# Optimization experiments

Measured on AMD Instinct MI355X. Metric: run time of the kernel, lower is better.

The kernel has to match this reference:

```python
import jax, jax.numpy as jnp
import numpy as np

S = 512          # number of scenes (sequences)
P = 128          # pedestrians per scene
G = 16           # groups per scene (labels 1..G, each of size P//G)
D_IN, D_HID, D_OUT, D_FINAL = 256, 512, 16, 64


def setup_inputs() -> dict:
    key = jax.random.key(0)
    ks = jax.random.split(key, 10)
    B = S * P
    h_states = jax.random.normal(ks[0], (B, D_IN), dtype=jnp.float32)
    end_pos = jax.random.normal(ks[1], (B, 2), dtype=jnp.float32)
    starts = jnp.arange(S, dtype=jnp.int64) * P
    seq_start_end = jnp.stack([starts, starts + P], axis=1)
    # labels 1..G within each scene; every group present -> n_group = G (static)
    end_group = ((jnp.arange(B, dtype=jnp.int64) % G) + 1).reshape(B, 1)
    s = 0.05  # scale randn params to keep activations tame
    W_intra_0 = s * jax.random.normal(ks[2], (D_IN, D_HID), dtype=jnp.float32)
    W_intra_1 = s * jax.random.normal(ks[3], (D_HID, D_OUT), dtype=jnp.float32)
    W_inter_0 = s * jax.random.normal(ks[4], (D_OUT, D_HID), dtype=jnp.float32)
    W_inter_1 = s * jax.random.normal(ks[5], (D_HID, D_OUT), dtype=jnp.float32)
    out_W = s * jax.random.normal(ks[6], (2 * D_OUT, D_FINAL), dtype=jnp.float32)
    out_b = jnp.zeros((D_FINAL,), dtype=jnp.float32)
    return {"h_states": h_states, "end_pos": end_pos,
            "seq_start_end": seq_start_end, "end_group": end_group,
            "W_intra_0": W_intra_0, "W_intra_1": W_intra_1,
            "W_inter_0": W_inter_0, "W_inter_1": W_inter_1,
            "out_W": out_W, "out_b": out_b}


def reference(h_states, end_pos, seq_start_end, end_group,
              W_intra_0, W_intra_1, W_inter_0, W_inter_1, out_W, out_b):
    B = h_states.shape[0]
    num_seq = seq_start_end.shape[0]
    P_ = B // num_seq
    labels = end_group.reshape(num_seq, P_)
    h_seq = h_states.reshape(num_seq, P_, -1)
    eye = jnp.eye(P_, dtype=bool)
    grp_ids = jnp.arange(1, G + 1)

    def per_scene(h, lab):
        # intra-group adjacency: same nonzero group, plus self loops
        M = ((lab[:, None] == lab[None, :]) & (lab[:, None] != 0)) | eye
        Mf = M.astype(h.dtype)
        A = Mf / jnp.sum(Mf, axis=1, keepdims=True)          # row-normalize
        H = jax.nn.relu((A @ h) @ W_intra_0)
        H_intra = jax.nn.relu((A @ H) @ W_intra_1)           # (P, D_OUT)
        # GPool: unique rows of M == one-hot group membership (all labels nonzero)
        onehot = (lab[None, :] == grp_ids[:, None]).astype(h.dtype)  # (G, P)
        R = onehot / jnp.sum(onehot, axis=1, keepdims=True)
        Hg = R @ H_intra                                     # (G, D_OUT)
        # inter-group GCN over fully-connected normalized adjacency
        Ai = jnp.full((G, G), 1.0 / G, dtype=h.dtype)
        Hg = jax.nn.relu((Ai @ Hg) @ W_inter_0)
        Hg = jax.nn.relu((Ai @ Hg) @ W_inter_1)
        H_inter = R.T @ Hg                                   # GUnpool: (P, D_OUT)
        cat = jnp.concatenate([H_intra, H_inter], axis=1)    # (P, 2*D_OUT)
        return cat @ out_W + out_b

    out = jax.vmap(per_scene)(h_seq, labels)
    return out.reshape(B, -1)
```

## Files before the change

kernel.cpp:

```cpp
#include <hip/hip_runtime.h>
#include <hip/hip_bf16.h>

#define S_SCENES 512
#define P_PED    128
#define G_GRP    16
#define D_IN     256
#define D_HID    512
#define D_OUT    16
#define D_FINAL  64

typedef __bf16 bf16x8 __attribute__((ext_vector_type(8)));
typedef float  f32x4  __attribute__((ext_vector_type(4)));

#define HGS 264
#define Y1S 520

__device__ __forceinline__ float bf2f(unsigned short u) {
  unsigned int x = ((unsigned int)u) << 16;
  float f; __builtin_memcpy(&f, &x, 4); return f;
}
__device__ __forceinline__ unsigned short f2bf(float f) {
  unsigned int x; __builtin_memcpy(&x, &f, 4);
  unsigned int r = x + 0x7FFFu + ((x >> 16) & 1u);
  return (unsigned short)(r >> 16);
}

__global__ void build_wfrag(const float* __restrict__ W0,
                            const float* __restrict__ W1,
                            unsigned short* __restrict__ W0F,
                            unsigned short* __restrict__ W1F) {
  int tid = blockIdx.x * blockDim.x + threadIdx.x;
  if (tid < 131072) {
    int k = tid >> 9, n = tid & 511;
    float v = W0[tid];
    int k8 = k >> 5, kr = k & 31;
    int j = kr & 7, lhi = kr >> 3;
    int nt = n >> 4, n16 = n & 15;
    int l = lhi * 16 + n16;
    W0F[(((k8 * 32 + nt) * 64) + l) * 8 + j] = f2bf(v);
  } else {
    int t2 = tid - 131072;
    if (t2 < 8192) {
      int k = t2 >> 4, n = t2 & 15;
      float v = W1[t2];
      int ks = k >> 5, kr = k & 31;
      int j = kr & 7, lhi = kr >> 3;
      int l = lhi * 16 + n;
      W1F[((ks * 64) + l) * 8 + j] = f2bf(v);
    }
  }
}

__global__ __launch_bounds__(512, 4) void scene_kernel(
    const float* __restrict__ h,
    const int* __restrict__ sse,
    const int* __restrict__ grp,
    const unsigned short* __restrict__ W0F,
    const unsigned short* __restrict__ W1F,
    const float* __restrict__ Wi0,
    const float* __restrict__ Wi1,
    const float* __restrict__ Wout,
    const float* __restrict__ bout,
    float* __restrict__ out)
{
  __shared__ __align__(16) unsigned short y1[16 * Y1S];
  __shared__ __align__(16) unsigned short hg[G_GRP * HGS];
  __shared__ __align__(16) float hg2p[8 * 16 * 16];
  __shared__ __align__(16) float t1v[D_HID];
  __shared__ __align__(16) float orow[16 * D_FINAL];
  __shared__ int lab[P_PED];
  __shared__ int cnt[G_GRP];
  __shared__ int bad;
  __shared__ unsigned char members[G_GRP][P_PED];
  __shared__ float hg2[G_GRP][D_OUT];
  __shared__ float mvec[D_OUT];
  __shared__ float hiv[D_OUT];
  __shared__ float cvec[D_FINAL];

  const int t = threadIdx.x;
  const int s = blockIdx.x;
  const int is64 = (grp[1] == 0) ? 1 : 0;
  const int start = is64 ? sse[4 * s] : sse[2 * s];
  const int w = t >> 6;
  const int l = t & 63;
  const int m16 = l & 15;
  const int q = l >> 4;

  if (t < G_GRP) cnt[t] = 0;
  if (t == 0) bad = 0;
  __syncthreads();

  const float* hbase = h + (size_t)start * D_IN + (l << 2);
  f32x4 vbuf[8];
  #pragma unroll
  for (int j = 0; j < 8; ++j)
    vbuf[j] = *(const f32x4*)(hbase + (size_t)(w + 8 * j) * D_IN);

  int myg = -1;
  if (t < P_PED) {
    int idx = start + t;
    myg = (is64 ? grp[2 * idx] : grp[idx]) - 1;
  }
  if (t < P_PED) {
    if (myg != (t & 15)) atomicOr(&bad, 1);
    int g = myg;
    if (g < 0) g = 0; if (g > G_GRP - 1) g = G_GRP - 1;
    lab[t] = g;
    int slot = atomicAdd(&cnt[g], 1);
    if (slot < P_PED) members[g][slot] = (unsigned char)t;
  }

  f32x4 acc0 = {0.f, 0.f, 0.f, 0.f}, acc1 = {0.f, 0.f, 0.f, 0.f};
  #pragma unroll
  for (int j = 0; j < 8; ++j) {
    if (j & 1) acc1 += vbuf[j]; else acc0 += vbuf[j];
  }
  #pragma unroll
  for (int j = 0; j < 8; ++j)
    vbuf[j] = *(const f32x4*)(hbase + (size_t)(w + 8 * (j + 8)) * D_IN);
  #pragma unroll
  for (int j = 0; j < 8; ++j) {
    if (j & 1) acc1 += vbuf[j]; else acc0 += vbuf[j];
  }
  __syncthreads();

  {
    int g0 = w, g1 = w + 8;
    if (bad == 0) {
      acc0 *= 0.125f;
      acc1 *= 0.125f;
    } else {
      int cn0 = cnt[g0], cn1 = cnt[g1];
      acc0 = (f32x4){0.f, 0.f, 0.f, 0.f};
      acc1 = (f32x4){0.f, 0.f, 0.f, 0.f};
      for (int m = 0; m < cn0; ++m)
        acc0 += *(const f32x4*)(h + (size_t)(start + members[g0][m]) * D_IN + (l << 2));
      for (int m = 0; m < cn1; ++m)
        acc1 += *(const f32x4*)(h + (size_t)(start + members[g1][m]) * D_IN + (l << 2));
      acc0 *= 1.0f / (float)(cn0 > 0 ? cn0 : 1);
      acc1 *= 1.0f / (float)(cn1 > 0 ? cn1 : 1);
    }
    ushort4 o0, o1;
    o0.x = f2bf(acc0[0]); o0.y = f2bf(acc0[1]); o0.z = f2bf(acc0[2]); o0.w = f2bf(acc0[3]);
    o1.x = f2bf(acc1[0]); o1.y = f2bf(acc1[1]); o1.z = f2bf(acc1[2]); o1.w = f2bf(acc1[3]);
    *(ushort4*)&hg[g0 * HGS + (l << 2)] = o0;
    *(ushort4*)&hg[g1 * HGS + (l << 2)] = o1;
  }
  __syncthreads();

  bf16x8 afr[8];
  #pragma unroll
  for (int k8 = 0; k8 < 8; ++k8)
    afr[k8] = *(const bf16x8*)&hg[m16 * HGS + k8 * 32 + q * 8];

  #pragma unroll
  for (int ntl = 0; ntl < 4; ++ntl) {
    int nt = w * 4 + ntl;
    f32x4 acc = {0.f, 0.f, 0.f, 0.f};
    #pragma unroll
    for (int k8 = 0; k8 < 8; ++k8) {
      bf16x8 bfr = *(const bf16x8*)(W0F + (size_t)(((k8 * 32 + nt) * 64) + l) * 8);
      acc = __builtin_amdgcn_mfma_f32_16x16x32_bf16(afr[k8], bfr, acc, 0, 0, 0);
    }
    #pragma unroll
    for (int r = 0; r < 4; ++r) {
      float v = acc[r];
      v = v > 0.f ? v : 0.f;
      y1[(q * 4 + r) * Y1S + nt * 16 + m16] = f2bf(v);
    }
  }
  __syncthreads();

  {
    f32x4 acc = {0.f, 0.f, 0.f, 0.f};
    #pragma unroll
    for (int kk = 0; kk < 2; ++kk) {
      int ks = w * 2 + kk;
      bf16x8 a2 = *(const bf16x8*)&y1[m16 * Y1S + ks * 32 + q * 8];
      bf16x8 b2 = *(const bf16x8*)(W1F + (size_t)(ks * 64 + l) * 8);
      acc = __builtin_amdgcn_mfma_f32_16x16x32_bf16(a2, b2, acc, 0, 0, 0);
    }
    #pragma unroll
    for (int r = 0; r < 4; ++r)
      hg2p[(w * 16 + (q * 4 + r)) * 16 + m16] = acc[r];
  }
  __syncthreads();
  if (t < 256) {
    int g = t >> 4, n = t & 15;
    float sum = 0.f;
    #pragma unroll
    for (int ww = 0; ww < 8; ++ww) sum += hg2p[(ww * 16 + g) * 16 + n];
    hg2[g][n] = sum > 0.f ? sum : 0.f;
  }
  __syncthreads();

  if (t < D_OUT) {
    float sm = 0.f;
    #pragma unroll
    for (int g = 0; g < G_GRP; ++g) sm += hg2[g][t];
    mvec[t] = sm * (1.0f / 16.0f);
  }
  __syncthreads();
  {
    float sm = 0.f;
    #pragma unroll
    for (int n = 0; n < D_OUT; ++n) sm += mvec[n] * Wi0[n * D_HID + t];
    t1v[t] = sm > 0.f ? sm : 0.f;
  }
  __syncthreads();
  #pragma unroll
  for (int nn = 0; nn < 2; ++nn) {
    int n = w * 2 + nn;
    float part = 0.f;
    #pragma unroll
    for (int r = 0; r < 8; ++r) {
      int j = l + r * 64;
      part += t1v[j] * Wi1[j * D_OUT + n];
    }
    for (int off = 32; off; off >>= 1) part += __shfl_down(part, off);
    if (l == 0) hiv[n] = part > 0.f ? part : 0.f;
  }
  __syncthreads();
  if (t < D_FINAL) {
    float sm = 0.f;
    #pragma unroll
    for (int n = 0; n < D_OUT; ++n)
      sm += hiv[n] * Wout[(G_GRP + n) * D_FINAL + t];
    cvec[t] = sm;
  }
  __syncthreads();

  for (int it = 0; it < 2; ++it) {
    int item = t + it * 512;
    int g = item >> 6, c = item & 63;
    float sm = 0.f;
    #pragma unroll
    for (int n = 0; n < D_OUT; ++n)
      sm += hg2[g][n] * Wout[n * D_FINAL + c];
    int cn = cnt[g];
    float inv = 1.0f / (float)(cn > 0 ? cn : 1);
    sm += cvec[c] * inv + bout[c];
    orow[g * D_FINAL + c] = sm;
  }
  __syncthreads();

  for (int it = 0; it < 4; ++it) {
    int i4 = t + it * 512;
    int p  = i4 >> 4;
    int c4 = i4 & 15;
    int g  = lab[p];
    float4 v = *(const float4*)&orow[g * D_FINAL + c4 * 4];
    *(float4*)(out + (size_t)(start + p) * D_FINAL + c4 * 4) = v;
  }
}

extern "C" void kernel_launch(void* const* d_in, const int* in_sizes, int n_in,
                              void* d_out, int out_size, void* d_ws, size_t ws_size,
                              hipStream_t stream) {
  const float* h    = (const float*)d_in[0];
  const int*   sse  = (const int*)d_in[2];
  const int*   grp  = (const int*)d_in[3];
  const float* W0   = (const float*)d_in[4];
  const float* W1   = (const float*)d_in[5];
  const float* Wi0  = (const float*)d_in[6];
  const float* Wi1  = (const float*)d_in[7];
  const float* Wout = (const float*)d_in[8];
  const float* bout = (const float*)d_in[9];

  unsigned short* W0F = (unsigned short*)d_ws;
  unsigned short* W1F = (unsigned short*)d_ws + 131072;

  build_wfrag<<<544, 256, 0, stream>>>(W0, W1, W0F, W1F);
  scene_kernel<<<S_SCENES, 512, 0, stream>>>(h, sse, grp, W0F, W1F,
                                             Wi0, Wi1, Wout, bout,
                                             (float*)d_out);
}
```

Measured before the change: 129.1 us.

## Move group-mean reduction of h into wide prep kernel

Moves the per-scene group averaging of h_states (the 64MB streaming read) from the scene kernel into the prep kernel, which now runs 2048 small blocks for this work alongside the weight fragment build. The means are written as bf16 into workspace, and the scene kernel loads the 16x256 tile into LDS. This spreads the bandwidth-bound read over more blocks for better memory-level parallelism and takes register pressure off the large kernel. The cost is an extra round trip through workspace. The prep kernel assumes the regular label layout, so the scene kernel still recomputes the means from members when labels are irregular.

```diff
diff --git a/kernel.cpp b/kernel.cpp
--- a/kernel.cpp
+++ b/kernel.cpp
@@ -11,6 +11,7 @@
 
 typedef __bf16 bf16x8 __attribute__((ext_vector_type(8)));
 typedef float  f32x4  __attribute__((ext_vector_type(4)));
+typedef unsigned short u16x8 __attribute__((ext_vector_type(8)));
 
 #define HGS 264
 #define Y1S 520
@@ -25,28 +26,59 @@
   return (unsigned short)(r >> 16);
 }
 
-__global__ void build_wfrag(const float* __restrict__ W0,
-                            const float* __restrict__ W1,
-                            unsigned short* __restrict__ W0F,
-                            unsigned short* __restrict__ W1F) {
-  int tid = blockIdx.x * blockDim.x + threadIdx.x;
-  if (tid < 131072) {
-    int k = tid >> 9, n = tid & 511;
-    float v = W0[tid];
-    int k8 = k >> 5, kr = k & 31;
-    int j = kr & 7, lhi = kr >> 3;
-    int nt = n >> 4, n16 = n & 15;
-    int l = lhi * 16 + n16;
-    W0F[(((k8 * 32 + nt) * 64) + l) * 8 + j] = f2bf(v);
+__global__ __launch_bounds__(256, 8) void prep_kernel(
+    const float* __restrict__ h,
+    const int* __restrict__ sse,
+    const int* __restrict__ grp,
+    const float* __restrict__ W0,
+    const float* __restrict__ W1,
+    unsigned short* __restrict__ W0F,
+    unsigned short* __restrict__ W1F,
+    unsigned short* __restrict__ M)
+{
+  const int b = blockIdx.x;
+  const int t = threadIdx.x;
+  if (b < 4 * S_SCENES) {
+    const int s  = b >> 2;
+    const int q4 = b & 3;
+    const int is64 = (grp[1] == 0) ? 1 : 0;
+    const int start = is64 ? sse[4 * s] : sse[2 * s];
+    const int g  = t >> 4;
+    const int ci = t & 15;
+    const int col = q4 * 64 + ci * 4;
+    const float* base = h + (size_t)(start + g) * D_IN + col;
+    f32x4 v[8];
+    #pragma unroll
+    for (int m = 0; m < 8; ++m)
+      v[m] = *(const f32x4*)(base + (size_t)(16 * m) * D_IN);
+    f32x4 acc = {0.f, 0.f, 0.f, 0.f};
+    #pragma unroll
+    for (int m = 0; m < 8; ++m) acc += v[m];
+    acc *= 0.125f;
+    ushort4 o;
+    o.x = f2bf(acc[0]); o.y = f2bf(acc[1]);
+    o.z = f2bf(acc[2]); o.w = f2bf(acc[3]);
+    *(ushort4*)&M[(size_t)(s * G_GRP + g) * D_IN + col] = o;
   } else {
-    int t2 = tid - 131072;
-    if (t2 < 8192) {
-      int k = t2 >> 4, n = t2 & 15;
-      float v = W1[t2];
-      int ks = k >> 5, kr = k & 31;
+    int tid = (b - 4 * S_SCENES) * 256 + t;
+    if (tid < 131072) {
+      int k = tid >> 9, n = tid & 511;
+      float v = W0[tid];
+      int k8 = k >> 5, kr = k & 31;
       int j = kr & 7, lhi = kr >> 3;
-      int l = lhi * 16 + n;
-      W1F[((ks * 64) + l) * 8 + j] = f2bf(v);
+      int nt = n >> 4, n16 = n & 15;
+      int l = lhi * 16 + n16;
+      W0F[(((k8 * 32 + nt) * 64) + l) * 8 + j] = f2bf(v);
+    } else {
+      int t2 = tid - 131072;
+      if (t2 < 8192) {
+        int k = t2 >> 4, n = t2 & 15;
+        float v = W1[t2];
+        int ks = k >> 5, kr = k & 31;
+        int j = kr & 7, lhi = kr >> 3;
+        int l = lhi * 16 + n;
+        W1F[((ks * 64) + l) * 8 + j] = f2bf(v);
+      }
     }
   }
 }
@@ -57,6 +89,7 @@
     const int* __restrict__ grp,
     const unsigned short* __restrict__ W0F,
     const unsigned short* __restrict__ W1F,
+    const unsigned short* __restrict__ M,
     const float* __restrict__ Wi0,
     const float* __restrict__ Wi1,
     const float* __restrict__ Wout,
@@ -90,18 +123,15 @@
   if (t == 0) bad = 0;
   __syncthreads();
 
-  const float* hbase = h + (size_t)start * D_IN + (l << 2);
-  f32x4 vbuf[8];
-  #pragma unroll
-  for (int j = 0; j < 8; ++j)
-    vbuf[j] = *(const f32x4*)(hbase + (size_t)(w + 8 * j) * D_IN);
-
-  int myg = -1;
+  {
+    int g = t >> 5, ch = t & 31;
+    u16x8 v = *(const u16x8*)&M[(size_t)(s * G_GRP + g) * D_IN + ch * 8];
+    *(u16x8*)&hg[g * HGS + ch * 8] = v;
+  }
+
   if (t < P_PED) {
     int idx = start + t;
-    myg = (is64 ? grp[2 * idx] : grp[idx]) - 1;
-  }
-  if (t < P_PED) {
+    int myg = (is64 ? grp[2 * idx] : grp[idx]) - 1;
     if (myg != (t & 15)) atomicOr(&bad, 1);
     int g = myg;
     if (g < 0) g = 0; if (g > G_GRP - 1) g = G_GRP - 1;
@@ -109,44 +139,25 @@
     int slot = atomicAdd(&cnt[g], 1);
     if (slot < P_PED) members[g][slot] = (unsigned char)t;
   }
-
-  f32x4 acc0 = {0.f, 0.f, 0.f, 0.f}, acc1 = {0.f, 0.f, 0.f, 0.f};
-  #pragma unroll
-  for (int j = 0; j < 8; ++j) {
-    if (j & 1) acc1 += vbuf[j]; else acc0 += vbuf[j];
-  }
-  #pragma unroll
-  for (int j = 0; j < 8; ++j)
-    vbuf[j] = *(const f32x4*)(hbase + (size_t)(w + 8 * (j + 8)) * D_IN);
-  #pragma unroll
-  for (int j = 0; j < 8; ++j) {
-    if (j & 1) acc1 += vbuf[j]; else acc0 += vbuf[j];
-  }
-  __syncthreads();
-
-  {
+  __syncthreads();
+
+  if (bad != 0) {
     int g0 = w, g1 = w + 8;
-    if (bad == 0) {
-      acc0 *= 0.125f;
-      acc1 *= 0.125f;
-    } else {
-      int cn0 = cnt[g0], cn1 = cnt[g1];
-      acc0 = (f32x4){0.f, 0.f, 0.f, 0.f};
-      acc1 = (f32x4){0.f, 0.f, 0.f, 0.f};
-      for (int m = 0; m < cn0; ++m)
-        acc0 += *(const f32x4*)(h + (size_t)(start + members[g0][m]) * D_IN + (l << 2));
-      for (int m = 0; m < cn1; ++m)
-        acc1 += *(const f32x4*)(h + (size_t)(start + members[g1][m]) * D_IN + (l << 2));
-      acc0 *= 1.0f / (float)(cn0 > 0 ? cn0 : 1);
-      acc1 *= 1.0f / (float)(cn1 > 0 ? cn1 : 1);
-    }
+    int cn0 = cnt[g0], cn1 = cnt[g1];
+    f32x4 a0 = {0.f, 0.f, 0.f, 0.f}, a1 = {0.f, 0.f, 0.f, 0.f};
+    for (int m = 0; m < cn0; ++m)
+      a0 += *(const f32x4*)(h + (size_t)(start + members[g0][m]) * D_IN + (l << 2));
+    for (int m = 0; m < cn1; ++m)
+      a1 += *(const f32x4*)(h + (size_t)(start + members[g1][m]) * D_IN + (l << 2));
+    a0 *= 1.0f / (float)(cn0 > 0 ? cn0 : 1);
+    a1 *= 1.0f / (float)(cn1 > 0 ? cn1 : 1);
     ushort4 o0, o1;
-    o0.x = f2bf(acc0[0]); o0.y = f2bf(acc0[1]); o0.z = f2bf(acc0[2]); o0.w = f2bf(acc0[3]);
-    o1.x = f2bf(acc1[0]); o1.y = f2bf(acc1[1]); o1.z = f2bf(acc1[2]); o1.w = f2bf(acc1[3]);
+    o0.x = f2bf(a0[0]); o0.y = f2bf(a0[1]); o0.z = f2bf(a0[2]); o0.w = f2bf(a0[3]);
+    o1.x = f2bf(a1[0]); o1.y = f2bf(a1[1]); o1.z = f2bf(a1[2]); o1.w = f2bf(a1[3]);
     *(ushort4*)&hg[g0 * HGS + (l << 2)] = o0;
     *(ushort4*)&hg[g1 * HGS + (l << 2)] = o1;
-  }
-  __syncthreads();
+    __syncthreads();
+  }
 
   bf16x8 afr[8];
   #pragma unroll
@@ -269,9 +280,11 @@
 
   unsigned short* W0F = (unsigned short*)d_ws;
   unsigned short* W1F = (unsigned short*)d_ws + 131072;
-
-  build_wfrag<<<544, 256, 0, stream>>>(W0, W1, W0F, W1F);
-  scene_kernel<<<S_SCENES, 512, 0, stream>>>(h, sse, grp, W0F, W1F,
+  unsigned short* M   = (unsigned short*)d_ws + 139264;
+
+  prep_kernel<<<4 * S_SCENES + 544, 256, 0, stream>>>(h, sse, grp, W0, W1,
+                                                      W0F, W1F, M);
+  scene_kernel<<<S_SCENES, 512, 0, stream>>>(h, sse, grp, W0F, W1F, M,
                                              Wi0, Wi1, Wout, bout,
                                              (float*)d_out);
 }
```

New measurement: 135.2 us. 1.05x slower.
